# Optimization experiments

Measured on AMD Instinct MI355X. Metric: run time of the kernel, lower is better.

Reference implementation:

```python
import jax, jax.numpy as jnp
import numpy as np

B, S, E = 2, 2048, 2048
H, KVH, D = 16, 4, 128
GROUPS = H // KVH
WINDOW = 1024
CAP = 50.0
ROPE_BASE = 10000.0
RMS_EPS = 1e-6
LN_EPS = 1e-5

def setup_inputs() -> dict:
    key = jax.random.key(0)
    ks = jax.random.split(key, 5)
    return {
        "x": jax.random.normal(ks[0], (B, S, E), jnp.float32),
        "Wq": jax.random.normal(ks[1], (E, E), jnp.float32) * (1.0 / np.sqrt(E)),
        "Wk": jax.random.normal(ks[2], (KVH * D, E), jnp.float32) * (1.0 / np.sqrt(E)),
        "Wv": jax.random.normal(ks[3], (KVH * D, E), jnp.float32) * (1.0 / np.sqrt(E)),
        "Wo": jax.random.normal(ks[4], (E, E), jnp.float32) * (1.0 / np.sqrt(E * H)),
        "q_norm_w": jnp.ones((D,), jnp.float32),
        "k_norm_w": jnp.ones((D,), jnp.float32),
        "ln_gamma": jnp.ones((E,), jnp.float32),
        "ln_beta": jnp.zeros((E,), jnp.float32),
    }

def _rmsnorm(t, w):
    # normalize over last (head) dim
    var = jnp.mean(jnp.square(t), axis=-1, keepdims=True)
    return t * jax.lax.rsqrt(var + RMS_EPS) * w

def _rope(t):
    # t: [B, h, S, D]; rotate-half RoPE
    half = D // 2
    inv_freq = 1.0 / (ROPE_BASE ** (jnp.arange(0, D, 2, dtype=jnp.float32) / D))  # [D/2]
    ang = jnp.arange(S, dtype=jnp.float32)[:, None] * inv_freq[None, :]  # [S, D/2]
    cos = jnp.concatenate([jnp.cos(ang), jnp.cos(ang)], axis=-1)  # [S, D]
    sin = jnp.concatenate([jnp.sin(ang), jnp.sin(ang)], axis=-1)
    t1, t2 = t[..., :half], t[..., half:]
    rot = jnp.concatenate([-t2, t1], axis=-1)
    return t * cos + rot * sin

def reference(x, Wq, Wk, Wv, Wo, q_norm_w, k_norm_w, ln_gamma, ln_beta):
    b, s, _ = x.shape
    q = (x @ Wq.T).reshape(b, s, H, D).transpose(0, 2, 1, 3)    # [B,H,S,D]
    k = (x @ Wk.T).reshape(b, s, KVH, D).transpose(0, 2, 1, 3)  # [B,KVH,S,D]
    v = (x @ Wv.T).reshape(b, s, KVH, D).transpose(0, 2, 1, 3)
    # QK-RMSNorm (Gemma/PaLM2 style), then RoPE
    q = _rope(_rmsnorm(q, q_norm_w))
    k = _rope(_rmsnorm(k, k_norm_w))
    # GQA: repeat KV heads to match query heads
    k = jnp.repeat(k, GROUPS, axis=1)  # [B,H,S,D]
    v = jnp.repeat(v, GROUPS, axis=1)
    scores = jnp.einsum('bhqd,bhkd->bhqk', q, k) / jnp.sqrt(jnp.asarray(D, x.dtype))
    # tanh logit softcap (Gemma2)
    scores = CAP * jnp.tanh(scores / CAP)
    # causal + sliding-window mask: attend to j with 0 <= i-j < WINDOW
    i = jnp.arange(s)[:, None]
    j = jnp.arange(s)[None, :]
    mask = (j <= i) & ((i - j) < WINDOW)  # [S,S]
    neg = jnp.finfo(scores.dtype).min
    scores = jnp.where(mask[None, None], scores, neg)
    attn = jax.nn.softmax(scores, axis=-1)
    out = jnp.einsum('bhqk,bhkd->bhqd', attn, v)  # [B,H,S,D]
    out = out.transpose(0, 2, 1, 3).reshape(b, s, E) @ Wo.T
    # residual + LayerNorm (post-norm)
    y = x + out
    mu = jnp.mean(y, axis=-1, keepdims=True)
    var = jnp.var(y, axis=-1, keepdims=True)
    return (y - mu) * jax.lax.rsqrt(var + LN_EPS) * ln_gamma + ln_beta
```

## Files before the change

### kernel.cpp

```cpp
#include <hip/hip_runtime.h>
#include <stdint.h>

typedef __attribute__((ext_vector_type(8))) short short8;
typedef __attribute__((ext_vector_type(4))) float f32x4;
typedef unsigned short u16;
typedef unsigned int u32;

#define NTOK 4096
#define E 2048
#define S 2048
#define NH 16
#define NKVH 4
#define HD 128
#define NQKV 3072

__device__ __forceinline__ float bf2f(u16 u) {
    return __uint_as_float(((u32)u) << 16);
}
__device__ __forceinline__ u16 f2bf(float f) {
    u32 u = __float_as_uint(f);
    u32 r = (u + 0x7fffu + ((u >> 16) & 1u)) >> 16;
    return (u16)r;
}
__device__ __forceinline__ void gload_lds16(const u16* g, u16* l) {
    __builtin_amdgcn_global_load_lds(
        (const __attribute__((address_space(1))) unsigned int*)(g),
        (__attribute__((address_space(3))) unsigned int*)(l), 16, 0, 0);
}

__global__ void cast5(const float* __restrict__ x, const float* __restrict__ wq,
                      const float* __restrict__ wk, const float* __restrict__ wv,
                      const float* __restrict__ wo,
                      u16* __restrict__ xb, u16* __restrict__ wqkvb,
                      u16* __restrict__ wob) {
    int i = blockIdx.x * 256 + threadIdx.x;
    const float* s; u16* d; int rel;
    if (i < 2097152)      { s = x;  d = xb;  rel = i; }
    else if (i < 3145728) { s = wq; d = wqkvb; rel = i - 2097152; }
    else if (i < 3407872) { s = wk; d = wqkvb + 4194304; rel = i - 3145728; }
    else if (i < 3670016) { s = wv; d = wqkvb + 5242880; rel = i - 3407872; }
    else                  { s = wo; d = wob; rel = i - 3670016; }
    float4 v = *(const float4*)(s + (size_t)rel * 4);
    ushort4 o;
    o.x = f2bf(v.x); o.y = f2bf(v.y); o.z = f2bf(v.z); o.w = f2bf(v.w);
    *(ushort4*)(d + (size_t)rel * 4) = o;
}

#define LADDR(row, ko) ((row) * 64 + ((ko) ^ (((row) & 7) << 3)))
#define GSB   __builtin_amdgcn_sched_barrier(0)
#define GBAR  __builtin_amdgcn_s_barrier()
#define LGKM0 do { asm volatile("s_waitcnt lgkmcnt(0)" ::: "memory"); GSB; } while (0)

__device__ __forceinline__ void stage1(u16* lds, const u16* g, int row0,
                                       int kt, int K, int tid) {
    const int rr = tid >> 3;
    const int chunk = (tid & 7) ^ (rr & 7);
    gload_lds16(g + (size_t)(row0 + rr) * K + kt + chunk * 8,
                lds + (row0 + (tid >> 6) * 8) * 64);
}

__global__ __launch_bounds__(512, 2)
void gemm_qkv(const u16* __restrict__ A, const u16* __restrict__ Bt,
              float* __restrict__ C, int M, int N, int K) {
    __shared__ u16 As2[2 * 8192];
    __shared__ u16 Bs2[2 * 12288];
    const int tid = threadIdx.x;
    const int w = tid >> 6, lane = tid & 63;
    const int lr = lane & 15, quad = lane >> 4;
    const int qo = quad * 8;
    const int wr = w >> 2, wc = w & 3;
    const int am = wr * 64;
    const int bn = wc * 48;

    const int nbx = N / 192;
    int wg = blockIdx.x;
    {
        const int nwg = gridDim.x;
        const int q = nwg >> 3, r = nwg & 7;
        const int xcd = wg & 7, loc = wg >> 3;
        wg = (xcd < r ? xcd * (q + 1) : r * (q + 1) + (xcd - r) * q) + loc;
    }
    const int n0 = (wg % nbx) * 192;
    const int m0 = (wg / nbx) * 128;

    const u16* gA = A + (size_t)m0 * K;
    const u16* gB = Bt + (size_t)n0 * K;
    const int nt = K >> 6;

    f32x4 acc[4][3];
#pragma unroll
    for (int mi = 0; mi < 4; mi++)
#pragma unroll
        for (int ni = 0; ni < 3; ni++)
            acc[mi][ni] = (f32x4){0.f, 0.f, 0.f, 0.f};

    short8 af[4][2], bf[3][2];

    stage1(As2, gA, 0, 0, K, tid);
    stage1(As2, gA, 64, 0, K, tid);
#pragma unroll
    for (int r = 0; r < 3; r++) stage1(Bs2, gB, r * 64, 0, K, tid);
    if (nt > 1) {
        stage1(As2 + 8192, gA, 0, 64, K, tid);
        stage1(As2 + 8192, gA, 64, 64, K, tid);
        stage1(Bs2 + 12288, gB, 0, 64, K, tid);
        stage1(Bs2 + 12288, gB, 64, 64, K, tid);
        asm volatile("s_waitcnt vmcnt(4)" ::: "memory");
    } else {
        asm volatile("s_waitcnt vmcnt(0)" ::: "memory");
    }
    GSB; GBAR;

    for (int t = 0; t < nt; ++t) {
        const int pb = t & 1;
        u16* Ap = As2 + pb * 8192;
        u16* Bp = Bs2 + pb * 12288;
        u16* Bn = Bs2 + (pb ^ 1) * 12288;
        const int kt1 = (t + 1) << 6, kt2 = (t + 2) << 6;

#pragma unroll
        for (int mi = 0; mi < 4; mi++)
#pragma unroll
            for (int kk = 0; kk < 2; kk++)
                af[mi][kk] = *(const short8*)&Ap[LADDR(am + mi * 16 + lr, kk * 32 + qo)];
#pragma unroll
        for (int ni = 0; ni < 3; ni++)
#pragma unroll
            for (int kk = 0; kk < 2; kk++)
                bf[ni][kk] = *(const short8*)&Bp[LADDR(bn + ni * 16 + lr, kk * 32 + qo)];
        if (t + 1 < nt) stage1(Bn, gB, 128, kt1, K, tid);
        GSB; GBAR; LGKM0;
        __builtin_amdgcn_s_setprio(1);
#pragma unroll
        for (int mi = 0; mi < 4; mi++)
#pragma unroll
            for (int ni = 0; ni < 3; ni++)
#pragma unroll
                for (int kk = 0; kk < 2; kk++)
                    acc[mi][ni] = __builtin_amdgcn_mfma_f32_16x16x32_bf16(
                        af[mi][kk], bf[ni][kk], acc[mi][ni], 0, 0, 0);
        __builtin_amdgcn_s_setprio(0);
        if (t + 2 < nt) {
            stage1(Ap, gA, 0, kt2, K, tid);
            stage1(Ap, gA, 64, kt2, K, tid);
            stage1(Bp, gB, 0, kt2, K, tid);
            stage1(Bp, gB, 64, kt2, K, tid);
        }
        if (t + 2 >= nt) {
            asm volatile("s_waitcnt vmcnt(0)" ::: "memory");
        } else {
            asm volatile("s_waitcnt vmcnt(4)" ::: "memory");
        }
        GSB; GBAR;
    }

#pragma unroll
    for (int mi = 0; mi < 4; mi++)
#pragma unroll
        for (int ni = 0; ni < 3; ni++) {
            const int row = m0 + am + mi * 16 + quad * 4;
            const int col = n0 + bn + ni * 16 + lr;
            f32x4 v = acc[mi][ni];
            C[(size_t)(row + 0) * N + col] = v[0];
            C[(size_t)(row + 1) * N + col] = v[1];
            C[(size_t)(row + 2) * N + col] = v[2];
            C[(size_t)(row + 3) * N + col] = v[3];
        }
}

__global__ __launch_bounds__(512, 2)
void gemm_proj(const u16* __restrict__ A, const u16* __restrict__ Bt,
               float* __restrict__ C, int M, int N, int K) {
    __shared__ u16 As2[2 * 8192];
    __shared__ u16 Bs2[2 * 8192];
    const int tid = threadIdx.x;
    const int w = tid >> 6, lane = tid & 63;
    const int lr = lane & 15, quad = lane >> 4;
    const int qo = quad * 8;
    const int wr = w >> 2, wc = w & 3;
    const int am = wr * 64;
    const int bn = wc * 32;

    const int nbx = N >> 7;
    int wg = blockIdx.x;
    {
        const int nwg = gridDim.x;
        const int q = nwg >> 3, r = nwg & 7;
        const int xcd = wg & 7, loc = wg >> 3;
        wg = (xcd < r ? xcd * (q + 1) : r * (q + 1) + (xcd - r) * q) + loc;
    }
    const int n0 = (wg % nbx) << 7;
    const int m0 = (wg / nbx) << 7;

    const u16* gA = A + (size_t)m0 * K;
    const u16* gB = Bt + (size_t)n0 * K;
    const int nt = K >> 6;

    f32x4 acc[4][2];
#pragma unroll
    for (int mi = 0; mi < 4; mi++)
#pragma unroll
        for (int ni = 0; ni < 2; ni++)
            acc[mi][ni] = (f32x4){0.f, 0.f, 0.f, 0.f};

    short8 af[4][2], bf[2][2];

    stage1(As2, gA, 0, 0, K, tid);
    stage1(As2, gA, 64, 0, K, tid);
    stage1(Bs2, gB, 0, 0, K, tid);
    stage1(Bs2, gB, 64, 0, K, tid);
    if (nt > 1) {
        stage1(As2 + 8192, gA, 0, 64, K, tid);
        stage1(As2 + 8192, gA, 64, 64, K, tid);
        stage1(Bs2 + 8192, gB, 0, 64, K, tid);
        asm volatile("s_waitcnt vmcnt(3)" ::: "memory");
    } else {
        asm volatile("s_waitcnt vmcnt(0)" ::: "memory");
    }
    GSB; GBAR;

    for (int t = 0; t < nt; ++t) {
        const int pb = t & 1;
        u16* Ap = As2 + pb * 8192;
        u16* Bp = Bs2 + pb * 8192;
        u16* Bn = Bs2 + (pb ^ 1) * 8192;
        const int kt1 = (t + 1) << 6, kt2 = (t + 2) << 6;

#pragma unroll
        for (int mi = 0; mi < 4; mi++)
#pragma unroll
            for (int kk = 0; kk < 2; kk++)
                af[mi][kk] = *(const short8*)&Ap[LADDR(am + mi * 16 + lr, kk * 32 + qo)];
#pragma unroll
        for (int ni = 0; ni < 2; ni++)
#pragma unroll
            for (int kk = 0; kk < 2; kk++)
                bf[ni][kk] = *(const short8*)&Bp[LADDR(bn + ni * 16 + lr, kk * 32 + qo)];
        if (t + 1 < nt) stage1(Bn, gB, 64, kt1, K, tid);
        GSB; GBAR; LGKM0;
        __builtin_amdgcn_s_setprio(1);
#pragma unroll
        for (int mi = 0; mi < 4; mi++)
#pragma unroll
            for (int ni = 0; ni < 2; ni++)
#pragma unroll
                for (int kk = 0; kk < 2; kk++)
                    acc[mi][ni] = __builtin_amdgcn_mfma_f32_16x16x32_bf16(
                        af[mi][kk], bf[ni][kk], acc[mi][ni], 0, 0, 0);
        __builtin_amdgcn_s_setprio(0);
        if (t + 2 < nt) {
            stage1(Ap, gA, 0, kt2, K, tid);
            stage1(Ap, gA, 64, kt2, K, tid);
            stage1(Bp, gB, 0, kt2, K, tid);
        }
        if (t + 2 >= nt) {
            asm volatile("s_waitcnt vmcnt(0)" ::: "memory");
        } else {
            asm volatile("s_waitcnt vmcnt(3)" ::: "memory");
        }
        GSB; GBAR;
    }

#pragma unroll
    for (int mi = 0; mi < 4; mi++)
#pragma unroll
        for (int ni = 0; ni < 2; ni++) {
            const int row = m0 + am + mi * 16 + quad * 4;
            const int col = n0 + bn + ni * 16 + lr;
            f32x4 v = acc[mi][ni];
            C[(size_t)(row + 0) * N + col] = v[0];
            C[(size_t)(row + 1) * N + col] = v[1];
            C[(size_t)(row + 2) * N + col] = v[2];
            C[(size_t)(row + 3) * N + col] = v[3];
        }
}

#define LDT 65
#define RMSBLKS 20480
__global__ __launch_bounds__(256)
void prep(const float* __restrict__ qkv,
          const float* __restrict__ qw, const float* __restrict__ kw,
          u16* __restrict__ qdst, u16* __restrict__ kdst, u16* __restrict__ vdst) {
    __shared__ u16 Ts[128 * LDT];
    if (blockIdx.x < RMSBLKS) {
        int p = blockIdx.x * 4 + (threadIdx.x >> 6);
        int lane = threadIdx.x & 63;
        const float* src; const float* w; u16* dst; int HH;
        if (p < NTOK * NH) { src = qkv; w = qw; dst = qdst; HH = NH; }
        else { p -= NTOK * NH; src = qkv + 2048; w = kw; dst = kdst; HH = NKVH; }
        int n = p / HH;
        int h = p - n * HH;
        int b = n >> 11;
        int s = n & 2047;
        const float* row = src + (size_t)n * NQKV + h * HD;
        float t1 = row[lane];
        float t2 = row[lane + 64];
        float ss = t1 * t1 + t2 * t2;
#pragma unroll
        for (int o = 1; o < 64; o <<= 1) ss += __shfl_xor(ss, o);
        float r = rsqrtf(ss * (1.f / 128.f) + 1e-6f);
        float a1 = t1 * r * w[lane];
        float a2 = t2 * r * w[lane + 64];
        float freq = expf(lane * -0.14391156831212787f);
        float ang = (float)s * freq;
        float sn, cs;
        sincosf(ang, &sn, &cs);
        float o1 = a1 * cs - a2 * sn;
        float o2 = a2 * cs + a1 * sn;
        size_t base = (((size_t)(b * HH + h)) * S + s) * HD;
        dst[base + lane] = f2bf(o1);
        dst[base + 64 + lane] = f2bf(o2);
    } else {
        const int idx = blockIdx.x - RMSBLKS;
        const int t = threadIdx.x;
        const int s0 = (idx & 31) * 64;
        const int kh = (idx >> 5) & 3;
        const int b = idx >> 7;
        const float* base = qkv + ((size_t)(b * S + s0)) * NQKV + 2560 + kh * HD;
#pragma unroll
        for (int i = 0; i < 8; i++) {
            int ii = i * 256 + t;
            int r = ii >> 5, c4 = (ii & 31) * 4;
            float4 v = *(const float4*)(base + (size_t)r * NQKV + c4);
            Ts[(c4 + 0) * LDT + r] = f2bf(v.x);
            Ts[(c4 + 1) * LDT + r] = f2bf(v.y);
            Ts[(c4 + 2) * LDT + r] = f2bf(v.z);
            Ts[(c4 + 3) * LDT + r] = f2bf(v.w);
        }
        __syncthreads();
        u16* obase = vdst + ((size_t)(b * NKVH + kh) * HD) * S + s0;
#pragma unroll
        for (int i = 0; i < 4; i++) {
            int ii = i * 256 + t;
            int d = ii >> 3, s8 = (ii & 7) * 8;
            const u16* row = &Ts[d * LDT + s8];
            short8 o;
#pragma unroll
            for (int j = 0; j < 8; j++) o[j] = (short)row[j];
            *(short8*)(obase + (size_t)d * S + s8) = o;
        }
    }
}

#define KSX(key, cb) ((key) * 128 + ((((cb) ^ ((key) & 15))) * 8))
#define VSX(d, cb)   ((d) * 64 + ((((cb) ^ ((d) & 7))) * 8))
#define PSX(row, cb) ((row) * 64 + ((((cb) ^ ((row) & 7))) * 8))
#define QBLK 64

__global__ __launch_bounds__(256, 4)
void attn_mfma(const u16* __restrict__ qa, const u16* __restrict__ ka,
               const u16* __restrict__ vt, u16* __restrict__ out) {
    __shared__ u16 Ks[64 * 128];
    __shared__ u16 Vs[128 * 64];
    __shared__ u16 Ps[64 * 64];
    const int tid = threadIdx.x;
    const int w = tid >> 6, lane = tid & 63;
    const int lr = lane & 15, quad = lane >> 4;

    const int bid = blockIdx.x;
    const int g = bid >> 8, p = bid & 255;
    const int j = p >> 5, hb = p & 31;
    int qt;
    if (g == 0) qt = 31 - j;
    else if (g == 1) qt = 23 - j;
    else if (g == 2) qt = 8 + j;
    else qt = 7 - j;
    const int h = hb >> 1, b = hb & 1;
    const int kh = h >> 2;
    const int q0 = qt * QBLK;
    const int qg0 = q0 + w * 16;

    const float KQK = 0.0051006974f;
    const float KP  = -144.26950408889634f;

    const u16* kbase0 = ka + (((size_t)(b * NKVH + kh)) * S) * HD;
    const u16* vtbase0 = vt + ((size_t)(b * NKVH + kh) * HD) * S;

    short8 qf[4];
    {
        const u16* qrow = qa + (((size_t)(b * NH + h)) * S + qg0 + lr) * HD;
#pragma unroll
        for (int c = 0; c < 4; c++)
            qf[c] = *(const short8*)(qrow + c * 32 + quad * 8);
    }

    f32x4 O[8];
#pragma unroll
    for (int dt = 0; dt < 8; dt++) O[dt] = (f32x4){0.f, 0.f, 0.f, 0.f};
    float l[4] = {0.f, 0.f, 0.f, 0.f};

    const int jt0 = (q0 >= 1024) ? (q0 - 1024) : 0;
    const int jtend = q0;
    const int qmin = qg0, qmax = qg0 + 15;

    for (int jt = jt0; jt <= jtend; jt += 64) {
        const u16* kbase = kbase0 + (size_t)jt * HD;
        const u16* vtbase = vtbase0 + jt;
        __syncthreads();
#pragma unroll
        for (int i = 0; i < 4; i++) {
            int idx = i * 256 + tid;
            int key = idx >> 4, cbk = (idx & 15) ^ (key & 15);
            gload_lds16(kbase + (size_t)key * HD + cbk * 8,
                        &Ks[(i * 256 + w * 64) * 8]);
            int dd = idx >> 3, cbv = (idx & 7) ^ (dd & 7);
            gload_lds16(vtbase + (size_t)dd * S + cbv * 8,
                        &Vs[(i * 256 + w * 64) * 8]);
        }
        __syncthreads();

        u16* Pw = &Ps[w * 16 * 64];
        bool any = false;

#pragma unroll
        for (int kt = 0; kt < 4; kt++) {
            const int keymin = jt + kt * 16;
            bool need = (keymin <= qmax) && (keymin + 15 >= qmin - 1023);
            bool full = (keymin + 15 <= qmin) && (keymin >= qmax - 1023);
            if (need) {
                any = true;
                f32x4 a = (f32x4){0.f, 0.f, 0.f, 0.f};
                __builtin_amdgcn_s_setprio(1);
#pragma unroll
                for (int c = 0; c < 4; c++) {
                    short8 kf = *(const short8*)(&Ks[KSX(kt * 16 + lr, 4 * c + quad)]);
                    a = __builtin_amdgcn_mfma_f32_16x16x32_bf16(qf[c], kf, a, 0, 0, 0);
                }
                __builtin_amdgcn_s_setprio(0);
#pragma unroll
                for (int r = 0; r < 4; r++) {
                    float t = __builtin_amdgcn_exp2f(a[r] * KQK);
                    float p2 = __builtin_amdgcn_exp2f(
                        KP * __builtin_amdgcn_rcpf(t + 1.f));
                    if (!full) {
                        int rel = keymin + lr - (qg0 + quad * 4 + r);
                        bool valid = (rel <= 0) && (rel > -1024);
                        p2 = valid ? p2 : 0.f;
                    }
                    l[r] += p2;
                    Pw[PSX(quad * 4 + r, kt * 2 + (lr >> 3)) + (lr & 7)] =
                        (u16)(__float_as_uint(p2) >> 16);
                }
            } else {
#pragma unroll
                for (int r = 0; r < 4; r++)
                    Pw[PSX(quad * 4 + r, kt * 2 + (lr >> 3)) + (lr & 7)] = 0;
            }
        }

        if (any) {
            __builtin_amdgcn_s_setprio(1);
#pragma unroll
            for (int c2 = 0; c2 < 2; c2++) {
                short8 pf = *(const short8*)(&Pw[PSX(lr, c2 * 4 + quad)]);
#pragma unroll
                for (int dt = 0; dt < 8; dt++) {
                    short8 vf = *(const short8*)(&Vs[VSX(dt * 16 + lr, c2 * 4 + quad)]);
                    O[dt] = __builtin_amdgcn_mfma_f32_16x16x32_bf16(pf, vf, O[dt], 0, 0, 0);
                }
            }
            __builtin_amdgcn_s_setprio(0);
        }
    }

#pragma unroll
    for (int r = 0; r < 4; r++) {
        l[r] += __shfl_xor(l[r], 1);
        l[r] += __shfl_xor(l[r], 2);
        l[r] += __shfl_xor(l[r], 4);
        l[r] += __shfl_xor(l[r], 8);
    }
#pragma unroll
    for (int r = 0; r < 4; r++) {
        float inv = 1.f / l[r];
        u16* orow = out + ((size_t)(b * S + qg0 + quad * 4 + r)) * E + h * HD;
#pragma unroll
        for (int dt = 0; dt < 8; dt++)
            orow[dt * 16 + lr] = f2bf(O[dt][r] * inv);
    }
}

__global__ __launch_bounds__(256)
void ln_kernel(const float* __restrict__ x, const float* __restrict__ pr,
               const float* __restrict__ g, const float* __restrict__ be,
               float* __restrict__ out) {
    int n = blockIdx.x;
    int tid = threadIdx.x;
    const float* xr = x + (size_t)n * E;
    const float* p = pr + (size_t)n * E;
    float y[8];
    float s = 0.f, ss = 0.f;
#pragma unroll
    for (int i = 0; i < 2; i++) {
        float4 a = *(const float4*)(xr + tid * 8 + i * 4);
        float4 b = *(const float4*)(p + tid * 8 + i * 4);
        float v0 = a.x + b.x, v1 = a.y + b.y, v2 = a.z + b.z, v3 = a.w + b.w;
        y[i * 4 + 0] = v0; y[i * 4 + 1] = v1; y[i * 4 + 2] = v2; y[i * 4 + 3] = v3;
        s += v0 + v1 + v2 + v3;
        ss += v0 * v0 + v1 * v1 + v2 * v2 + v3 * v3;
    }
#pragma unroll
    for (int o = 1; o < 64; o <<= 1) {
        s += __shfl_xor(s, o);
        ss += __shfl_xor(ss, o);
    }
    __shared__ float r0[4], r1[4];
    int w = tid >> 6;
    if ((tid & 63) == 0) { r0[w] = s; r1[w] = ss; }
    __syncthreads();
    s = r0[0] + r0[1] + r0[2] + r0[3];
    ss = r1[0] + r1[1] + r1[2] + r1[3];
    float mu = s * (1.f / 2048.f);
    float var = ss * (1.f / 2048.f) - mu * mu;
    float rs = rsqrtf(var + 1e-5f);
    float* orow = out + (size_t)n * E;
#pragma unroll
    for (int i = 0; i < 8; i++) {
        int c = tid * 8 + i;
        orow[c] = (y[i] - mu) * rs * g[c] + be[c];
    }
}

extern "C" void kernel_launch(void* const* d_in, const int* in_sizes, int n_in,
                              void* d_out, int out_size, void* d_ws, size_t ws_size,
                              hipStream_t stream) {
    (void)in_sizes; (void)n_in; (void)out_size; (void)ws_size;
    const float* x   = (const float*)d_in[0];
    const float* Wq  = (const float*)d_in[1];
    const float* Wk  = (const float*)d_in[2];
    const float* Wv  = (const float*)d_in[3];
    const float* Wo  = (const float*)d_in[4];
    const float* qnw = (const float*)d_in[5];
    const float* knw = (const float*)d_in[6];
    const float* lng = (const float*)d_in[7];
    const float* lnb = (const float*)d_in[8];
    float* out = (float*)d_out;

    char* ws = (char*)d_ws;
    size_t off = 0;
    auto alloc = [&](size_t bytes) -> char* {
        char* pp = ws + off;
        off = (off + bytes + 255) & ~(size_t)255;
        return pp;
    };
    u16*  xb     = (u16*)alloc((size_t)NTOK * E * 2);
    u16*  Wqkvb  = (u16*)alloc((size_t)NQKV * E * 2);
    u16*  Wob    = (u16*)alloc((size_t)E * E * 2);
    float* qkvraw= (float*)alloc((size_t)NTOK * NQKV * 4);
    u16*  qaa    = (u16*)alloc((size_t)NTOK * E * 2);
    u16*  kaa    = (u16*)alloc((size_t)NTOK * 512 * 2);
    u16*  vtt    = (u16*)alloc((size_t)NTOK * 512 * 2);
    u16*  attn_o = xb;
    float* proj  = qkvraw;

    cast5<<<dim3(18432), 256, 0, stream>>>(x, Wq, Wk, Wv, Wo, xb, Wqkvb, Wob);

    gemm_qkv<<<dim3(512), 512, 0, stream>>>(xb, Wqkvb, qkvraw, NTOK, NQKV, E);

    prep<<<dim3(RMSBLKS + 256), 256, 0, stream>>>(qkvraw, qnw, knw, qaa, kaa, vtt);

    attn_mfma<<<dim3(1024), 256, 0, stream>>>(qaa, kaa, vtt, attn_o);

    gemm_proj<<<dim3(512), 512, 0, stream>>>(attn_o, Wob, proj, NTOK, E, E);

    ln_kernel<<<dim3(NTOK), 256, 0, stream>>>(x, proj, lng, lnb, out);
}
```

Measured before the change: 296.0 us.

## Fuse Q RMSNorm+RoPE into attention and precompute RoPE cos/sin table

Q normalization and rotary embedding move out of the prep kernel into the attention kernel prologue. It reads raw fp32 Q from the QKV buffer, normalizes and rotates it, stages it through the K shared buffer, and loads fragments from there. This drops the bf16 Q intermediate write and read and shrinks prep to K and V only. A cos/sin table is computed once in extra blocks of the cast kernel, replacing per-element expf/sincosf with table lookups. The cost is more fp32 global traffic in the attention prologue and an extra barrier there.

```diff
diff --git a/kernel.cpp b/kernel.cpp
--- a/kernel.cpp
+++ b/kernel.cpp
@@ -28,11 +28,22 @@
         (__attribute__((address_space(3))) unsigned int*)(l), 16, 0, 0);
 }
 
+#define CASTBLKS 18432
 __global__ void cast5(const float* __restrict__ x, const float* __restrict__ wq,
                       const float* __restrict__ wk, const float* __restrict__ wv,
                       const float* __restrict__ wo,
                       u16* __restrict__ xb, u16* __restrict__ wqkvb,
-                      u16* __restrict__ wob) {
+                      u16* __restrict__ wob, float* __restrict__ tab) {
+    if (blockIdx.x >= CASTBLKS) {
+        int idx2 = (blockIdx.x - CASTBLKS) * 256 + threadIdx.x;
+        int sct = idx2 >> 6, ln2 = idx2 & 63;
+        float freq = expf(ln2 * -0.14391156831212787f);
+        float ang = (float)sct * freq;
+        float sn, cs;
+        sincosf(ang, &sn, &cs);
+        ((float2*)tab)[idx2] = (float2){cs, sn};
+        return;
+    }
     int i = blockIdx.x * 256 + threadIdx.x;
     const float* s; u16* d; int rel;
     if (i < 2097152)      { s = x;  d = xb;  rel = i; }
@@ -276,42 +287,36 @@
 }
 
 #define LDT 65
-#define RMSBLKS 20480
+#define KBLKS 4096
 __global__ __launch_bounds__(256)
-void prep(const float* __restrict__ qkv,
-          const float* __restrict__ qw, const float* __restrict__ kw,
-          u16* __restrict__ qdst, u16* __restrict__ kdst, u16* __restrict__ vdst) {
+void prep(const float* __restrict__ qkv, const float* __restrict__ kw,
+          const float* __restrict__ tab,
+          u16* __restrict__ kdst, u16* __restrict__ vdst) {
     __shared__ u16 Ts[128 * LDT];
-    if (blockIdx.x < RMSBLKS) {
+    if (blockIdx.x < KBLKS) {
         int p = blockIdx.x * 4 + (threadIdx.x >> 6);
         int lane = threadIdx.x & 63;
-        const float* src; const float* w; u16* dst; int HH;
-        if (p < NTOK * NH) { src = qkv; w = qw; dst = qdst; HH = NH; }
-        else { p -= NTOK * NH; src = qkv + 2048; w = kw; dst = kdst; HH = NKVH; }
-        int n = p / HH;
-        int h = p - n * HH;
+        int n = p >> 2;
+        int h = p & 3;
         int b = n >> 11;
         int s = n & 2047;
-        const float* row = src + (size_t)n * NQKV + h * HD;
+        const float* row = qkv + (size_t)n * NQKV + 2048 + h * HD;
         float t1 = row[lane];
         float t2 = row[lane + 64];
         float ss = t1 * t1 + t2 * t2;
 #pragma unroll
         for (int o = 1; o < 64; o <<= 1) ss += __shfl_xor(ss, o);
         float r = rsqrtf(ss * (1.f / 128.f) + 1e-6f);
-        float a1 = t1 * r * w[lane];
-        float a2 = t2 * r * w[lane + 64];
-        float freq = expf(lane * -0.14391156831212787f);
-        float ang = (float)s * freq;
-        float sn, cs;
-        sincosf(ang, &sn, &cs);
-        float o1 = a1 * cs - a2 * sn;
-        float o2 = a2 * cs + a1 * sn;
-        size_t base = (((size_t)(b * HH + h)) * S + s) * HD;
-        dst[base + lane] = f2bf(o1);
-        dst[base + 64 + lane] = f2bf(o2);
+        float a1 = t1 * r * kw[lane];
+        float a2 = t2 * r * kw[lane + 64];
+        float2 csn = ((const float2*)tab)[(s << 6) + lane];
+        float o1 = a1 * csn.x - a2 * csn.y;
+        float o2 = a2 * csn.x + a1 * csn.y;
+        size_t base = (((size_t)(b * NKVH + h)) * S + s) * HD;
+        kdst[base + lane] = f2bf(o1);
+        kdst[base + 64 + lane] = f2bf(o2);
     } else {
-        const int idx = blockIdx.x - RMSBLKS;
+        const int idx = blockIdx.x - KBLKS;
         const int t = threadIdx.x;
         const int s0 = (idx & 31) * 64;
         const int kh = (idx >> 5) & 3;
@@ -348,8 +353,10 @@
 #define QBLK 64
 
 __global__ __launch_bounds__(256, 4)
-void attn_mfma(const u16* __restrict__ qa, const u16* __restrict__ ka,
-               const u16* __restrict__ vt, u16* __restrict__ out) {
+void attn_mfma(const float* __restrict__ qkv, const float* __restrict__ qw,
+               const float* __restrict__ tab,
+               const u16* __restrict__ ka, const u16* __restrict__ vt,
+               u16* __restrict__ out) {
     __shared__ u16 Ks[64 * 128];
     __shared__ u16 Vs[128 * 64];
     __shared__ u16 Ps[64 * 64];
@@ -376,9 +383,54 @@
     const u16* kbase0 = ka + (((size_t)(b * NKVH + kh)) * S) * HD;
     const u16* vtbase0 = vt + ((size_t)(b * NKVH + kh) * HD) * S;
 
+    {
+        const int rowL = lane >> 2, q4 = lane & 3;
+        const int sl = w * 16 + rowL;
+        const int sg = q0 + sl;
+        const float* qr = qkv + ((size_t)(b * S + sg)) * NQKV + h * HD + q4 * 16;
+        float ss = 0.f;
+#pragma unroll
+        for (int c = 0; c < 4; c++) {
+            float4 u = *(const float4*)(qr + c * 4);
+            float4 vv = *(const float4*)(qr + 64 + c * 4);
+            ss += u.x * u.x + u.y * u.y + u.z * u.z + u.w * u.w;
+            ss += vv.x * vv.x + vv.y * vv.y + vv.z * vv.z + vv.w * vv.w;
+        }
+        ss += __shfl_xor(ss, 1);
+        ss += __shfl_xor(ss, 2);
+        const float rn = rsqrtf(ss * (1.f / 128.f) + 1e-6f);
+        u16* krow = &Ks[sl * 128 + q4 * 16];
+#pragma unroll
+        for (int c = 0; c < 4; c++) {
+            float4 u = *(const float4*)(qr + c * 4);
+            float4 vv = *(const float4*)(qr + 64 + c * 4);
+            float4 w1 = *(const float4*)(qw + q4 * 16 + c * 4);
+            float4 w2 = *(const float4*)(qw + 64 + q4 * 16 + c * 4);
+            ushort4 p1, p2;
+            const float* pu = (const float*)&u;
+            const float* pv = (const float*)&vv;
+            const float* pw1 = (const float*)&w1;
+            const float* pw2 = (const float*)&w2;
+            u16* d1 = (u16*)&p1;
+            u16* d2 = (u16*)&p2;
+#pragma unroll
+            for (int k = 0; k < 4; k++) {
+                int dd = q4 * 16 + c * 4 + k;
+                float2 csn = ((const float2*)tab)[(sg << 6) + dd];
+                float a1 = pu[k] * rn * pw1[k];
+                float a2 = pv[k] * rn * pw2[k];
+                d1[k] = f2bf(a1 * csn.x - a2 * csn.y);
+                d2[k] = f2bf(a2 * csn.x + a1 * csn.y);
+            }
+            *(ushort4*)(krow + c * 4) = p1;
+            *(ushort4*)(krow + 64 + c * 4) = p2;
+        }
+    }
+    __syncthreads();
+
     short8 qf[4];
     {
-        const u16* qrow = qa + (((size_t)(b * NH + h)) * S + qg0 + lr) * HD;
+        const u16* qrow = &Ks[(w * 16 + lr) * 128];
 #pragma unroll
         for (int c = 0; c < 4; c++)
             qf[c] = *(const short8*)(qrow + c * 32 + quad * 8);
@@ -547,19 +599,20 @@
     u16*  Wqkvb  = (u16*)alloc((size_t)NQKV * E * 2);
     u16*  Wob    = (u16*)alloc((size_t)E * E * 2);
     float* qkvraw= (float*)alloc((size_t)NTOK * NQKV * 4);
-    u16*  qaa    = (u16*)alloc((size_t)NTOK * E * 2);
     u16*  kaa    = (u16*)alloc((size_t)NTOK * 512 * 2);
     u16*  vtt    = (u16*)alloc((size_t)NTOK * 512 * 2);
+    float* tab   = (float*)alloc((size_t)S * 64 * 8);
     u16*  attn_o = xb;
     float* proj  = qkvraw;
 
-    cast5<<<dim3(18432), 256, 0, stream>>>(x, Wq, Wk, Wv, Wo, xb, Wqkvb, Wob);
+    cast5<<<dim3(CASTBLKS + 512), 256, 0, stream>>>(x, Wq, Wk, Wv, Wo, xb, Wqkvb,
+                                                    Wob, tab);
 
     gemm_qkv<<<dim3(512), 512, 0, stream>>>(xb, Wqkvb, qkvraw, NTOK, NQKV, E);
 
-    prep<<<dim3(RMSBLKS + 256), 256, 0, stream>>>(qkvraw, qnw, knw, qaa, kaa, vtt);
-
-    attn_mfma<<<dim3(1024), 256, 0, stream>>>(qaa, kaa, vtt, attn_o);
+    prep<<<dim3(KBLKS + 256), 256, 0, stream>>>(qkvraw, knw, tab, kaa, vtt);
+
+    attn_mfma<<<dim3(1024), 256, 0, stream>>>(qkvraw, qnw, tab, kaa, vtt, attn_o);
 
     gemm_proj<<<dim3(512), 512, 0, stream>>>(attn_o, Wob, proj, NTOK, E, E);
 
```

After: 290.9 us. About the same (-1.7%).
